# Performance work log

Measured on AMD Instinct MI355X. Metric: run time of the kernel, lower is better.

Reference implementation:

```python
import jax, jax.numpy as jnp
import numpy as np

BATCH, SEQ = 64, 64
D = 256            # model_dim (state = [h;c], each half = 128)
HALF = D // 2
VOCAB = 32000
MLP_DIM = 1024
NUM_CLASSES = 3


def setup_inputs() -> dict:
    key = jax.random.key(0)
    ks = jax.random.split(key, 12)
    s = lambda k, shp, fan: jax.random.normal(k, shp, jnp.float32) * (2.0 / fan) ** 0.5
    return {
        "sentences": jax.random.randint(ks[0], (BATCH, SEQ), 0, VOCAB, dtype=jnp.int64),
        "transitions": jnp.zeros((BATCH, 2 * SEQ - 2), dtype=jnp.int64),
        "emb": jax.random.normal(ks[1], (VOCAB, D), jnp.float32) * 0.1,
        "comp_W": s(ks[2], (2 * HALF, 5 * HALF), 2 * HALF),
        "comp_b": jnp.zeros((5 * HALF,), jnp.float32),
        "sel_w": s(ks[3], (D, 1), D),
        "sel_b": jnp.zeros((1,), jnp.float32),
        "mlp_w0": s(ks[4], (D, MLP_DIM), D),
        "mlp_b0": jnp.zeros((MLP_DIM,), jnp.float32),
        "mlp_w1": s(ks[5], (MLP_DIM, MLP_DIM), MLP_DIM),
        "mlp_b1": jnp.zeros((MLP_DIM,), jnp.float32),
        "cls_w": s(ks[6], (MLP_DIM, NUM_CLASSES), MLP_DIM),
        "cls_b": jnp.zeros((NUM_CLASSES,), jnp.float32),
    }


def _treelstm(left, right, comp_W, comp_b):
    # left/right: [B, L, D] state pairs = concat(h, c)
    hl, cl = left[..., :HALF], left[..., HALF:]
    hr, cr = right[..., :HALF], right[..., HALF:]
    a = jnp.concatenate([hl, hr], -1) @ comp_W + comp_b  # [B, L, 5*HALF]
    i, fl, fr, g, o = jnp.split(a, 5, axis=-1)
    c = (jax.nn.sigmoid(fl) * cl + jax.nn.sigmoid(fr) * cr
         + jax.nn.sigmoid(i) * jnp.tanh(g))
    h = jax.nn.sigmoid(o) * jnp.tanh(c)
    return jnp.concatenate([h, c], -1)  # [B, L, D]


def _pyramid(x, comp_W, comp_b, sel_w, sel_b):
    # x: [B, S, D] leaf states. Gated pyramid merge, eval mode (temperature=1).
    states = x
    for layer in range(SEQ - 1, 0, -1):
        left, right = states[:, :-1], states[:, 1:]      # [B, layer, D]
        comp = _treelstm(left, right, comp_W, comp_b)    # [B, layer, D]
        logits = (comp @ sel_w + sel_b)[..., 0]          # [B, layer]
        probs = jax.nn.softmax(logits, axis=-1)
        cs = jnp.cumsum(probs, axis=-1)
        copy_right = cs - probs                          # sum_{j<pos}
        rcs = jnp.flip(jnp.cumsum(jnp.flip(probs, -1), -1), -1)
        copy_left = rcs - probs                          # sum_{j>pos}
        states = (copy_left[..., None] * left
                  + copy_right[..., None] * right
                  + probs[..., None] * comp)
    return states[:, 0]  # [B, D]


def reference(sentences, transitions, emb, comp_W, comp_b, sel_w, sel_b,
              mlp_w0, mlp_b0, mlp_w1, mlp_b1, cls_w, cls_b):
    x = emb[sentences]                                   # [B, S, D]
    h = _pyramid(x, comp_W, comp_b, sel_w, sel_b)        # [B, D]
    z = jax.nn.relu(h @ mlp_w0 + mlp_b0)
    z = jax.nn.relu(z @ mlp_w1 + mlp_b1)
    return z @ cls_w + cls_b                             # [B, num_classes]
```

## Files before the change

kernel.cpp:

```cpp
#include <hip/hip_runtime.h>

#define SEQ 64
#define LOG2E 1.4426950408889634f

typedef _Float16 f16;
typedef _Float16 f16x8 __attribute__((ext_vector_type(8)));
typedef _Float16 f16x2 __attribute__((ext_vector_type(2)));
typedef float f32x4 __attribute__((ext_vector_type(4)));

__device__ __forceinline__ float exp2_(float x) {
#if __has_builtin(__builtin_amdgcn_exp2f)
  return __builtin_amdgcn_exp2f(x);
#else
  return __builtin_exp2f(x);
#endif
}
__device__ __forceinline__ float sigp_(float a) {
  return __builtin_amdgcn_rcpf(1.0f + exp2_(-a));
}
__device__ __forceinline__ float tanhp_(float a) {
  return 1.0f - 2.0f * __builtin_amdgcn_rcpf(1.0f + exp2_(a));
}
__device__ __forceinline__ float tanh_(float x) {
  return 1.0f - 2.0f * __builtin_amdgcn_rcpf(1.0f + exp2_(x * (2.0f * LOG2E)));
}

template<int CTRL, int RMASK>
__device__ __forceinline__ float dpp_add(float x) {
  const int t = __builtin_amdgcn_update_dpp(0, __float_as_int(x), CTRL, RMASK, 0xF, true);
  return x + __int_as_float(t);
}
template<int CTRL>
__device__ __forceinline__ float dpp_max(float x) {
  const int t = __builtin_amdgcn_update_dpp(0, __float_as_int(x), CTRL, 0xF, 0xF, true);
  return fmaxf(x, __int_as_float(t));
}
__device__ __forceinline__ float red16(float v) {
  v = dpp_add<0xB1, 0xF>(v);
  v = dpp_add<0x4E, 0xF>(v);
  v = dpp_add<0x124, 0xF>(v);
  v = dpp_add<0x128, 0xF>(v);
  return v;
}
__device__ __forceinline__ float lane63f(float v) {
  return __int_as_float(__builtin_amdgcn_readlane(__float_as_int(v), 63));
}

#define HROW 136

__device__ __forceinline__ f16x8 gatherB(const float* __restrict__ cW,
                                         int kk, int q, int wv, int quad, int l15,
                                         float sc) {
  const int col = (q * 8 + wv) * 16 + l15;
  const int kb  = kk * 32 + quad * 8;
  f16x8 v;
  #pragma unroll
  for (int j = 0; j < 8; ++j) v[j] = (f16)(cW[(kb + j) * 640 + col] * sc);
  return v;
}

#define BLDS_OFF 0
#define CS_OFF   98304
#define HS_OFF   132624
#define LGP_OFF  150304
#define PS_OFF   152352
#define CLS_OFF  152608
#define CRS_OFF  152864
#define DYN_LDS  153120

__global__ __launch_bounds__(512, 1) void pyramid_kernel(
    const int*   __restrict__ sentences,
    const float* __restrict__ emb,
    const float* __restrict__ cW,
    const float* __restrict__ cb, const float* __restrict__ selw, const float* __restrict__ selb,
    const float* __restrict__ w0, const float* __restrict__ b0,
    const float* __restrict__ cbias,
    f16* __restrict__ z0h, float* __restrict__ out)
{
  extern __shared__ __align__(16) char dyn[];
  f16x8* Blds = (f16x8*)(dyn + BLDS_OFF);
  float* cS   = (float*)(dyn + CS_OFF);
  f16*   hS   = (f16*)  (dyn + HS_OFF);
  float* lgp  = (float*)(dyn + LGP_OFF);
  float* pS   = (float*)(dyn + PS_OFF);
  float* clS  = (float*)(dyn + CLS_OFF);
  float* crS  = (float*)(dyn + CRS_OFF);

  const int tid  = threadIdx.x;
  const int b    = blockIdx.x;
  const int wv   = tid >> 6;
  const int lane = tid & 63;
  const int quad = lane >> 4;
  const int l15  = lane & 15;
  const int d    = wv * 16 + l15;

  if (b == 0 && tid < 192) out[tid] = cbias[tid % 3];

  #pragma unroll
  for (int s = 0; s < 12; ++s) {
    const int kk = (s < 4) ? (4 + s) : (s - 4);
    const int q  = (s < 4) ? 3 : 4;
    const float sc = (q == 3) ? (2.0f * LOG2E) : LOG2E;
    Blds[s * 512 + tid] = gatherB(cW, kk, q, wv, quad, l15, sc);
  }
  f16x8 Breg[28];
  #pragma unroll
  for (int kk = 0; kk < 8; ++kk)
    #pragma unroll
    for (int q = 0; q < 3; ++q)
      Breg[kk * 3 + q] = gatherB(cW, kk, q, wv, quad, l15, LOG2E);
  #pragma unroll
  for (int kk = 0; kk < 4; ++kk)
    Breg[24 + kk] = gatherB(cW, kk, 3, wv, quad, l15, 2.0f * LOG2E);

  {
    const int s = tid >> 3, part = tid & 7;
    const int row = sentences[b * SEQ + s];
    const float4* er = (const float4*)(emb + (size_t)row * 256 + part * 32);
    #pragma unroll
    for (int i4 = 0; i4 < 8; ++i4) {
      const float4 v = er[i4];
      const float vv[4] = {v.x, v.y, v.z, v.w};
      #pragma unroll
      for (int c = 0; c < 4; ++c) {
        const int f = part * 32 + i4 * 4 + c;
        if (f < 128) hS[s * HROW + f] = (f16)vv[c];
        else         cS[s * 132 + (f - 128)] = vv[c];
      }
    }
  }
  if (tid < HROW) hS[64 * HROW + tid] = (f16)0.f;
  if (tid < 132)  cS[64 * 132 + tid] = 0.f;
  __syncthreads();

  float bq[5];
  #pragma unroll
  for (int q = 0; q < 5; ++q)
    bq[q] = cb[q * 128 + d] * ((q == 3) ? (2.0f * LOG2E) : LOG2E);
  const float swh = selw[d], swc = selw[128 + d], selbv = selb[0];

  for (int W = 63; W >= 1; --W) {
    const int NMT = (W + 15) >> 4;
    float chF[4][4], ccF[4][4], vF[4][4];

    #pragma unroll
    for (int mt = 0; mt < 4; ++mt) if (mt < NMT) {
      f32x4 acc[5];
      #pragma unroll
      for (int q = 0; q < 5; ++q) acc[q] = (f32x4){bq[q], bq[q], bq[q], bq[q]};
      const int rb = (mt * 16 + l15) * HROW + quad * 8;
      #pragma unroll
      for (int kk = 0; kk < 8; ++kk) {
        const f16x8 av = *(const f16x8*)&hS[rb + (kk >> 2) * HROW + (kk & 3) * 32];
        #pragma unroll
        for (int q = 0; q < 3; ++q)
          acc[q] = __builtin_amdgcn_mfma_f32_16x16x32_f16(av, Breg[kk * 3 + q], acc[q], 0, 0, 0);
        const f16x8 b3 = (kk < 4) ? Breg[24 + kk] : Blds[(kk - 4) * 512 + tid];
        acc[3] = __builtin_amdgcn_mfma_f32_16x16x32_f16(av, b3, acc[3], 0, 0, 0);
        const f16x8 b4 = Blds[(4 + kk) * 512 + tid];
        acc[4] = __builtin_amdgcn_mfma_f32_16x16x32_f16(av, b4, acc[4], 0, 0, 0);
      }
      const int n0q = mt * 16 + quad * 4;
      if (n0q < W) {
        float c5[5];
        #pragma unroll
        for (int r = 0; r < 5; ++r) c5[r] = cS[(n0q + r) * 132 + d];
        #pragma unroll
        for (int r = 0; r < 4; ++r) {
          const float c = sigp_(acc[1][r]) * c5[r] + sigp_(acc[2][r]) * c5[r + 1]
                        + sigp_(acc[0][r]) * tanhp_(acc[3][r]);
          const float h = sigp_(acc[4][r]) * tanh_(c);
          ccF[mt][r] = c; chF[mt][r] = h;
          vF[mt][r] = red16(__builtin_fmaf(h, swh, c * swc));
        }
      }
    }
    if (l15 == 0) {
      #pragma unroll
      for (int mt = 0; mt < 4; ++mt) if (mt < NMT) {
        const int n0q = mt * 16 + quad * 4;
        if (n0q < W) {
          #pragma unroll
          for (int r = 0; r < 4; ++r) {
            const int n = n0q + r;
            if (n < W) lgp[(wv << 6) + n] = vF[mt][r];
          }
        }
      }
    }
    __syncthreads();

    {
      float lg = -3.0e38f;
      if (lane < W) {
        float s = selbv;
        #pragma unroll
        for (int dg = 0; dg < 8; ++dg) s += lgp[(dg << 6) + lane];
        lg = s;
      }
      float m = lg;
      m = dpp_max<0xB1>(m); m = dpp_max<0x4E>(m);
      m = dpp_max<0x124>(m); m = dpp_max<0x128>(m);
      m = dpp_max<0x142>(m); m = dpp_max<0x143>(m);
      m = lane63f(m);
      const float e = (lane < W) ? __expf(lg - m) : 0.f;
      float t = e;
      t = dpp_add<0xB1, 0xF>(t); t = dpp_add<0x4E, 0xF>(t);
      t = dpp_add<0x124, 0xF>(t); t = dpp_add<0x128, 0xF>(t);
      t = dpp_add<0x142, 0xF>(t); t = dpp_add<0x143, 0xF>(t);
      t = lane63f(t);
      const float p = e * __builtin_amdgcn_rcpf(t);
      float cs = p;
      cs = dpp_add<0x111, 0xF>(cs);
      cs = dpp_add<0x112, 0xF>(cs);
      cs = dpp_add<0x114, 0xF>(cs);
      cs = dpp_add<0x118, 0xF>(cs);
      cs = dpp_add<0x142, 0xA>(cs);
      cs = dpp_add<0x143, 0xC>(cs);
      const float T = lane63f(cs);
      if (lane < W) {
        pS[lane]  = p;
        clS[lane] = T - cs;
        crS[lane] = cs - p;
      }
    }

    #pragma unroll
    for (int mt = 0; mt < 4; ++mt) if (mt < NMT) {
      const int n0q = mt * 16 + quad * 4;
      if (n0q < W) {
        const f32x4 pv  = *(const f32x4*)&pS[n0q];
        const f32x4 clv = *(const f32x4*)&clS[n0q];
        const f32x4 crv = *(const f32x4*)&crS[n0q];
        float oh[5], c5[5];
        #pragma unroll
        for (int r = 0; r < 5; ++r) {
          oh[r] = (float)hS[(n0q + r) * HROW + d];
          c5[r] = cS[(n0q + r) * 132 + d];
        }
        #pragma unroll
        for (int r = 0; r < 4; ++r) {
          const int n = n0q + r;
          if (n < W) {
            const float nh = clv[r] * oh[r] + crv[r] * oh[r + 1] + pv[r] * chF[mt][r];
            const float nc = clv[r] * c5[r] + crv[r] * c5[r + 1] + pv[r] * ccF[mt][r];
            hS[n * HROW + d] = (f16)nh;
            cS[n * 132 + d] = nc;
          }
        }
      }
    }
    __syncthreads();
  }

  {
    const int c0 = 2 * tid;
    float a0 = 0.f, a1 = 0.f;
    #pragma unroll 8
    for (int k = 0; k < 128; ++k) {
      const float x  = (float)hS[k];
      const float2 w = *(const float2*)&w0[k * 1024 + c0];
      a0 = __builtin_fmaf(x, w.x, a0);
      a1 = __builtin_fmaf(x, w.y, a1);
    }
    #pragma unroll 8
    for (int k = 0; k < 128; ++k) {
      const float x  = cS[k];
      const float2 w = *(const float2*)&w0[(128 + k) * 1024 + c0];
      a0 = __builtin_fmaf(x, w.x, a0);
      a1 = __builtin_fmaf(x, w.y, a1);
    }
    f16x2 p;
    p[0] = (f16)fmaxf(a0 + b0[c0], 0.f);
    p[1] = (f16)fmaxf(a1 + b0[c0 + 1], 0.f);
    *(f16x2*)&z0h[b * 1024 + c0] = p;
  }
}

#define ZROW 264
__global__ __launch_bounds__(256) void z1_kernel(
    const f16* __restrict__ z0h, const float* __restrict__ w1,
    const float* __restrict__ b1, const float* __restrict__ cwt,
    float* __restrict__ out)
{
  __shared__ __align__(16) f16 ZL[64 * ZROW];
  __shared__ __align__(16) f16 WL[16 * ZROW];
  const int t    = threadIdx.x;
  const int wv   = t >> 6;
  const int lane = t & 63;
  const int quad = lane >> 4;
  const int l15  = lane & 15;
  const int c0   = blockIdx.x * 16;

  f32x4 acc = (f32x4){0.f, 0.f, 0.f, 0.f};
  for (int k0 = 0; k0 < 1024; k0 += 256) {
    __syncthreads();
    #pragma unroll
    for (int i = 0; i < 8; ++i) {
      const int idx8 = (t + i * 256) * 8;
      const int row  = idx8 >> 8;
      const int ko   = idx8 & 255;
      *(f16x8*)&ZL[row * ZROW + ko] = *(const f16x8*)&z0h[row * 1024 + k0 + ko];
    }
    #pragma unroll
    for (int i = 0; i < 4; ++i) {
      const int idx = i * 256 + t;
      const int kc  = idx >> 2;
      const int c4  = (idx & 3) * 4;
      const float4 w4 = *(const float4*)&w1[(size_t)(k0 + kc) * 1024 + c0 + c4];
      WL[(c4 + 0) * ZROW + kc] = (f16)w4.x;
      WL[(c4 + 1) * ZROW + kc] = (f16)w4.y;
      WL[(c4 + 2) * ZROW + kc] = (f16)w4.z;
      WL[(c4 + 3) * ZROW + kc] = (f16)w4.w;
    }
    __syncthreads();
    #pragma unroll
    for (int kk = 0; kk < 8; ++kk) {
      const f16x8 av = *(const f16x8*)&ZL[(wv * 16 + l15) * ZROW + kk * 32 + quad * 8];
      const f16x8 bv = *(const f16x8*)&WL[l15 * ZROW + kk * 32 + quad * 8];
      acc = __builtin_amdgcn_mfma_f32_16x16x32_f16(av, bv, acc, 0, 0, 0);
    }
  }

  const int col = c0 + l15;
  const float bias = b1[col];
  const float cw0 = cwt[col * 3], cw1 = cwt[col * 3 + 1], cw2 = cwt[col * 3 + 2];
  #pragma unroll
  for (int r = 0; r < 4; ++r) {
    const int row = wv * 16 + quad * 4 + r;
    const float z = fmaxf(acc[r] + bias, 0.f);
    const float p0 = red16(z * cw0);
    const float p1 = red16(z * cw1);
    const float p2 = red16(z * cw2);
    if (l15 == 0) {
      atomicAdd(&out[row * 3 + 0], p0);
      atomicAdd(&out[row * 3 + 1], p1);
      atomicAdd(&out[row * 3 + 2], p2);
    }
  }
}

extern "C" void kernel_launch(void* const* d_in, const int* in_sizes, int n_in,
                              void* d_out, int out_size, void* d_ws, size_t ws_size,
                              hipStream_t stream) {
  (void)in_sizes; (void)n_in; (void)out_size; (void)ws_size;
  f16* z0h = (f16*)d_ws;

  (void)hipFuncSetAttribute((const void*)pyramid_kernel,
                            hipFuncAttributeMaxDynamicSharedMemorySize, DYN_LDS);

  pyramid_kernel<<<dim3(64), dim3(512), DYN_LDS, stream>>>(
      (const int*)d_in[0],
      (const float*)d_in[2],
      (const float*)d_in[3],
      (const float*)d_in[4],
      (const float*)d_in[5],
      (const float*)d_in[6],
      (const float*)d_in[7],
      (const float*)d_in[8],
      (const float*)d_in[12],
      z0h, (float*)d_out);
  z1_kernel<<<dim3(64), dim3(256), 0, stream>>>(
      z0h,
      (const float*)d_in[9],
      (const float*)d_in[10],
      (const float*)d_in[11],
      (float*)d_out);
}
```

Baseline: 434.3 us.

## Fuse second MLP layer and classifier into the pyramid kernel tail

Removes the separate z1 kernel launch and the workspace round trip. Each pyramid block now computes its own row of the 1024x1024 MLP layer in fp32 FMA from an LDS vector, then applies the classifier with wave reductions and writes its output directly, with no atomics or bias pre-init. The cost is that each of the 64 blocks streams the full 4 MB w1 matrix (served mostly from L2/MALL) and uses scalar FMA instead of MFMA. This trades a kernel launch and a dependency gap for redundant weight reads.

```diff
diff --git a/kernel.cpp b/kernel.cpp
--- a/kernel.cpp
+++ b/kernel.cpp
@@ -40,6 +40,15 @@
   v = dpp_add<0x4E, 0xF>(v);
   v = dpp_add<0x124, 0xF>(v);
   v = dpp_add<0x128, 0xF>(v);
+  return v;
+}
+__device__ __forceinline__ float redwave(float v) {
+  v = dpp_add<0xB1, 0xF>(v);
+  v = dpp_add<0x4E, 0xF>(v);
+  v = dpp_add<0x124, 0xF>(v);
+  v = dpp_add<0x128, 0xF>(v);
+  v = dpp_add<0x142, 0xF>(v);
+  v = dpp_add<0x143, 0xF>(v);
   return v;
 }
 __device__ __forceinline__ float lane63f(float v) {
@@ -74,8 +83,9 @@
     const float* __restrict__ cW,
     const float* __restrict__ cb, const float* __restrict__ selw, const float* __restrict__ selb,
     const float* __restrict__ w0, const float* __restrict__ b0,
-    const float* __restrict__ cbias,
-    f16* __restrict__ z0h, float* __restrict__ out)
+    const float* __restrict__ w1, const float* __restrict__ b1,
+    const float* __restrict__ cwt, const float* __restrict__ clsb,
+    float* __restrict__ out)
 {
   extern __shared__ __align__(16) char dyn[];
   f16x8* Blds = (f16x8*)(dyn + BLDS_OFF);
@@ -94,8 +104,6 @@
   const int l15  = lane & 15;
   const int d    = wv * 16 + l15;
 
-  if (b == 0 && tid < 192) out[tid] = cbias[tid % 3];
-
   #pragma unroll
   for (int s = 0; s < 12; ++s) {
     const int kk = (s < 4) ? (4 + s) : (s - 4);
@@ -204,11 +212,7 @@
       m = dpp_max<0x142>(m); m = dpp_max<0x143>(m);
       m = lane63f(m);
       const float e = (lane < W) ? __expf(lg - m) : 0.f;
-      float t = e;
-      t = dpp_add<0xB1, 0xF>(t); t = dpp_add<0x4E, 0xF>(t);
-      t = dpp_add<0x124, 0xF>(t); t = dpp_add<0x128, 0xF>(t);
-      t = dpp_add<0x142, 0xF>(t); t = dpp_add<0x143, 0xF>(t);
-      t = lane63f(t);
+      const float t = lane63f(redwave(e));
       const float p = e * __builtin_amdgcn_rcpf(t);
       float cs = p;
       cs = dpp_add<0x111, 0xF>(cs);
@@ -253,6 +257,8 @@
     __syncthreads();
   }
 
+  f16* x1 = (f16*)(dyn + LGP_OFF);
+
   {
     const int c0 = 2 * tid;
     float a0 = 0.f, a1 = 0.f;
@@ -273,78 +279,47 @@
     f16x2 p;
     p[0] = (f16)fmaxf(a0 + b0[c0], 0.f);
     p[1] = (f16)fmaxf(a1 + b0[c0 + 1], 0.f);
-    *(f16x2*)&z0h[b * 1024 + c0] = p;
-  }
-}
-
-#define ZROW 264
-__global__ __launch_bounds__(256) void z1_kernel(
-    const f16* __restrict__ z0h, const float* __restrict__ w1,
-    const float* __restrict__ b1, const float* __restrict__ cwt,
-    float* __restrict__ out)
-{
-  __shared__ __align__(16) f16 ZL[64 * ZROW];
-  __shared__ __align__(16) f16 WL[16 * ZROW];
-  const int t    = threadIdx.x;
-  const int wv   = t >> 6;
-  const int lane = t & 63;
-  const int quad = lane >> 4;
-  const int l15  = lane & 15;
-  const int c0   = blockIdx.x * 16;
-
-  f32x4 acc = (f32x4){0.f, 0.f, 0.f, 0.f};
-  for (int k0 = 0; k0 < 1024; k0 += 256) {
-    __syncthreads();
-    #pragma unroll
-    for (int i = 0; i < 8; ++i) {
-      const int idx8 = (t + i * 256) * 8;
-      const int row  = idx8 >> 8;
-      const int ko   = idx8 & 255;
-      *(f16x8*)&ZL[row * ZROW + ko] = *(const f16x8*)&z0h[row * 1024 + k0 + ko];
-    }
-    #pragma unroll
-    for (int i = 0; i < 4; ++i) {
-      const int idx = i * 256 + t;
-      const int kc  = idx >> 2;
-      const int c4  = (idx & 3) * 4;
-      const float4 w4 = *(const float4*)&w1[(size_t)(k0 + kc) * 1024 + c0 + c4];
-      WL[(c4 + 0) * ZROW + kc] = (f16)w4.x;
-      WL[(c4 + 1) * ZROW + kc] = (f16)w4.y;
-      WL[(c4 + 2) * ZROW + kc] = (f16)w4.z;
-      WL[(c4 + 3) * ZROW + kc] = (f16)w4.w;
-    }
-    __syncthreads();
-    #pragma unroll
-    for (int kk = 0; kk < 8; ++kk) {
-      const f16x8 av = *(const f16x8*)&ZL[(wv * 16 + l15) * ZROW + kk * 32 + quad * 8];
-      const f16x8 bv = *(const f16x8*)&WL[l15 * ZROW + kk * 32 + quad * 8];
-      acc = __builtin_amdgcn_mfma_f32_16x16x32_f16(av, bv, acc, 0, 0, 0);
-    }
-  }
-
-  const int col = c0 + l15;
-  const float bias = b1[col];
-  const float cw0 = cwt[col * 3], cw1 = cwt[col * 3 + 1], cw2 = cwt[col * 3 + 2];
-  #pragma unroll
-  for (int r = 0; r < 4; ++r) {
-    const int row = wv * 16 + quad * 4 + r;
-    const float z = fmaxf(acc[r] + bias, 0.f);
-    const float p0 = red16(z * cw0);
-    const float p1 = red16(z * cw1);
-    const float p2 = red16(z * cw2);
-    if (l15 == 0) {
-      atomicAdd(&out[row * 3 + 0], p0);
-      atomicAdd(&out[row * 3 + 1], p1);
-      atomicAdd(&out[row * 3 + 2], p2);
-    }
+    *(f16x2*)&x1[c0] = p;
+  }
+  __syncthreads();
+
+  {
+    const int c0 = 2 * tid;
+    float a0 = 0.f, a1 = 0.f;
+    #pragma unroll 4
+    for (int k8 = 0; k8 < 128; ++k8) {
+      const f16x8 xv = *(const f16x8*)&x1[k8 * 8];
+      #pragma unroll
+      for (int j = 0; j < 8; ++j) {
+        const float x  = (float)xv[j];
+        const float2 w = *(const float2*)&w1[(size_t)(k8 * 8 + j) * 1024 + c0];
+        a0 = __builtin_fmaf(x, w.x, a0);
+        a1 = __builtin_fmaf(x, w.y, a1);
+      }
+    }
+    const float2 bb = *(const float2*)&b1[c0];
+    const float z0v = fmaxf(a0 + bb.x, 0.f);
+    const float z1v = fmaxf(a1 + bb.y, 0.f);
+    #pragma unroll
+    for (int j = 0; j < 3; ++j) {
+      float v = __builtin_fmaf(z0v, cwt[c0 * 3 + j], z1v * cwt[(c0 + 1) * 3 + j]);
+      v = lane63f(redwave(v));
+      if (lane == 0) pS[wv * 3 + j] = v;
+    }
+  }
+  __syncthreads();
+  if (tid < 3) {
+    float s = clsb[tid];
+    #pragma unroll
+    for (int w = 0; w < 8; ++w) s += pS[w * 3 + tid];
+    out[b * 3 + tid] = s;
   }
 }
 
 extern "C" void kernel_launch(void* const* d_in, const int* in_sizes, int n_in,
                               void* d_out, int out_size, void* d_ws, size_t ws_size,
                               hipStream_t stream) {
-  (void)in_sizes; (void)n_in; (void)out_size; (void)ws_size;
-  f16* z0h = (f16*)d_ws;
+  (void)in_sizes; (void)n_in; (void)out_size; (void)d_ws; (void)ws_size;
 
   (void)hipFuncSetAttribute((const void*)pyramid_kernel,
                             hipFuncAttributeMaxDynamicSharedMemorySize, DYN_LDS);
@@ -358,12 +333,9 @@
       (const float*)d_in[6],
       (const float*)d_in[7],
       (const float*)d_in[8],
-      (const float*)d_in[12],
-      z0h, (float*)d_out);
-  z1_kernel<<<dim3(64), dim3(256), 0, stream>>>(
-      z0h,
       (const float*)d_in[9],
       (const float*)d_in[10],
       (const float*)d_in[11],
+      (const float*)d_in[12],
       (float*)d_out);
 }
```

After: 476.6 us. 1.1x slower.
